# Performance work log

Measured on AMD Instinct MI355X. Metric: run time of the kernel, lower is better.

Reference implementation:

```python
import jax, jax.numpy as jnp
import numpy as np

B, H, W = 2, 64, 64
C = 19          # num_classes
D = 64          # embed_dim
NH = 4          # num_heads
E = 4           # num_experts
HD = 128        # hidden_dim = 2*D
EPS = 1e-5


def setup_inputs() -> dict:
    key = jax.random.key(0)
    ks = jax.random.split(key, 12)
    n = lambda k, shape, s=0.02: jax.random.normal(k, shape, jnp.float32) * s
    z = lambda shape: jnp.zeros(shape, jnp.float32)
    o = lambda shape: jnp.ones(shape, jnp.float32)
    return {
        "depth_map": jax.random.normal(ks[0], (B, 1, H, W), jnp.float32),
        "prob_map": jax.nn.softmax(jax.random.normal(ks[1], (B, C, H, W), jnp.float32), axis=1),
        "emb_w": n(ks[2], (1 + C, D)), "emb_b": z((D,)),            # 1x1 conv == per-pixel linear
        "in_proj_w": n(ks[3], (D, 3 * D)), "in_proj_b": z((3 * D,)),
        "attn_out_w": n(ks[4], (D, D)), "attn_out_b": z((D,)),
        "ln1_g": o((D,)), "ln1_b": z((D,)),
        "ln2_g": o((D,)), "ln2_b": z((D,)),
        "exp_w1": n(ks[5], (E, D, HD)), "exp_b1": z((E, HD)),
        "exp_w2": n(ks[6], (E, HD, D)), "exp_b2": z((E, D)),
        "gate_w": n(ks[7], (D, E)), "gate_b": z((E,)),
        "proj_w": n(ks[8], (D, 1)), "proj_b": z((1,)),
    }


def _layernorm(x, g, b):
    m = jnp.mean(x, axis=-1, keepdims=True)
    v = jnp.mean(jnp.square(x - m), axis=-1, keepdims=True)
    return (x - m) * jax.lax.rsqrt(v + EPS) * g + b


def reference(depth_map, prob_map, emb_w, emb_b, in_proj_w, in_proj_b,
              attn_out_w, attn_out_b, ln1_g, ln1_b, ln2_g, ln2_b,
              exp_w1, exp_b1, exp_w2, exp_b2, gate_w, gate_b, proj_w, proj_b):
    Bv, _, Hv, Wv = depth_map.shape
    N = Hv * Wv
    dh = D // NH

    x = jnp.concatenate([depth_map, prob_map], axis=1)            # [B, 1+C, H, W]
    # 1x1 conv embedding -> token sequence [B, N, D]
    x_seq = (jnp.einsum('bchw,cd->bhwd', x, emb_w) + emb_b).reshape(Bv, N, D)

    # pre-norm self-attention
    xn = _layernorm(x_seq, ln1_g, ln1_b)
    qkv = xn @ in_proj_w + in_proj_b                              # [B, N, 3D]
    q, k, v = jnp.split(qkv, 3, axis=-1)
    q = q.reshape(Bv, N, NH, dh)
    k = k.reshape(Bv, N, NH, dh)
    v = v.reshape(Bv, N, NH, dh)
    scores = jnp.einsum('bqhd,bkhd->bhqk', q, k) / np.sqrt(dh).astype(np.float32)
    attn = jax.nn.softmax(scores, axis=-1)
    o = jnp.einsum('bhqk,bkhd->bqhd', attn, v).reshape(Bv, N, D)
    attn_out = o @ attn_out_w + attn_out_b
    x_att = x_seq + attn_out

    # soft MoE over all tokens
    xn2 = _layernorm(x_att, ln2_g, ln2_b)
    gw = jax.nn.softmax(xn2 @ gate_w + gate_b, axis=-1)           # [B, N, E]
    h1 = jax.nn.relu(jnp.einsum('bnd,edh->bneh', xn2, exp_w1) + exp_b1)
    eo = jnp.einsum('bneh,ehd->bned', h1, exp_w2) + exp_b2        # [B, N, E, D]
    combined = jnp.einsum('bned,bne->bnd', eo, gw)
    x_out = x_att + combined

    weight_seq = x_out @ proj_w + proj_b                          # [B, N, 1]
    return jax.nn.sigmoid(weight_seq.reshape(Bv, 1, Hv, Wv))
```

## Files before the change

kernel.cpp:

```cpp
#include <hip/hip_runtime.h>
#include <math.h>

#define DEV __device__ __forceinline__

namespace {

constexpr int Bb  = 2;
constexpr int Nn  = 4096;
constexpr int Cc  = 19;
constexpr int NHh = 4;
constexpr int SEGS = 4;
constexpr float EPSv = 1e-5f;
constexpr float LOG2E = 1.4426950408889634f;

typedef __attribute__((ext_vector_type(4))) short short4v;
typedef __attribute__((ext_vector_type(8))) short short8v;
typedef __attribute__((ext_vector_type(4))) float f32x4;
typedef unsigned short ushort_t;
typedef unsigned int uint_t;

constexpr size_t QKV_F    = (size_t)Bb * Nn * 32;
constexpr size_t OFF_XSEQ = 0;
constexpr size_t OFF_XATT = OFF_XSEQ + (size_t)Bb*Nn*64;
constexpr size_t OFF_QB   = OFF_XATT + (size_t)Bb*Nn*64;
constexpr size_t OFF_KB   = OFF_QB + QKV_F;
constexpr size_t OFF_VB   = OFF_KB + QKV_F;
constexpr size_t OFF_VT   = OFF_VB + QKV_F;
constexpr size_t OFF_MP   = OFF_VT + QKV_F;
constexpr size_t OFF_LP   = OFF_MP + (size_t)Bb*NHh*SEGS*Nn;
constexpr size_t OFF_OP   = OFF_LP + (size_t)Bb*NHh*SEGS*Nn;
constexpr size_t OFF_XN2  = OFF_OP + (size_t)Bb*NHh*SEGS*Nn*16;
constexpr size_t OFF_GW   = OFF_XN2 + (size_t)Bb*Nn*32;
constexpr size_t OFF_H1   = OFF_GW + (size_t)Bb*Nn*4;
constexpr size_t OFF_W1T  = OFF_H1 + (size_t)Bb*Nn*256;
constexpr size_t OFF_W2T  = OFF_W1T + 16384;

DEV float wredsum(float x) {
  #pragma unroll
  for (int off = 32; off > 0; off >>= 1) x += __shfl_xor(x, off, 64);
  return x;
}
DEV ushort_t f2bf(float x) {
  uint_t u = __builtin_bit_cast(uint_t, x);
  u += 0x7fffu + ((u >> 16) & 1u);
  return (ushort_t)(u >> 16);
}
DEV uint_t cvtpk(float a, float b) {
  uint_t r;
  asm("v_cvt_pk_bf16_f32 %0, %1, %2" : "=v"(r) : "v"(a), "v"(b));
  return r;
}

__global__ __launch_bounds__(256) void k_wcvt(
    const float* __restrict__ w1, const float* __restrict__ w2,
    float* __restrict__ ws)
{
  const int idx = blockIdx.x * 256 + threadIdx.x;
  ushort_t* w1t = (ushort_t*)(ws + OFF_W1T);
  ushort_t* w2t = (ushort_t*)(ws + OFF_W2T);
  {
    const int col = idx >> 6, k = idx & 63;
    const int e = col >> 7, h = col & 127;
    w1t[idx] = f2bf(w1[((size_t)e * 64 + k) * 128 + h]);
  }
  {
    const int d = idx >> 9, kk = idx & 511;
    const int e = kk >> 7, h = kk & 127;
    w2t[idx] = f2bf(w2[((size_t)e * 128 + h) * 64 + d]);
  }
}

__global__ __launch_bounds__(256) void k_embed_qkv(
    const float* __restrict__ depth, const float* __restrict__ prob,
    const float* __restrict__ emb_w, const float* __restrict__ emb_b,
    const float* __restrict__ ipw,   const float* __restrict__ ipb,
    const float* __restrict__ ln1g,  const float* __restrict__ ln1b,
    float* __restrict__ ws)
{
  __shared__ float ipws[64 * 192];

  const int t = threadIdx.x;
  #pragma unroll
  for (int i = 0; i < 12; ++i) {
    const int idx = (i * 256 + t) * 4;
    *(float4*)&ipws[idx] = *(const float4*)&ipw[idx];
  }

  const int lane = t & 63;
  const int wid  = t >> 6;
  const int tok  = blockIdx.x * 4 + wid;
  const int b = tok >> 12, n = tok & (Nn - 1);
  const int d = lane;

  float acc = emb_b[d];
  acc += depth[(size_t)b * Nn + n] * emb_w[d];
  #pragma unroll
  for (int c = 0; c < Cc; ++c)
    acc += prob[((size_t)b * Cc + c) * Nn + n] * emb_w[(1 + c) * 64 + d];

  ws[OFF_XSEQ + (size_t)tok * 64 + d] = acc;

  float mean = wredsum(acc) * (1.f / 64.f);
  float diff = acc - mean;
  float var  = wredsum(diff * diff) * (1.f / 64.f);
  float xn   = diff * rsqrtf(var + EPSv) * ln1g[d] + ln1b[d];

  __syncthreads();

  float aq = ipb[d], ak = ipb[64 + d], av = ipb[128 + d];
  #pragma unroll 8
  for (int j = 0; j < 64; ++j) {
    float xj = __shfl(xn, j, 64);
    const float* wr = ipws + j * 192;
    aq = fmaf(xj, wr[d],       aq);
    ak = fmaf(xj, wr[64 + d],  ak);
    av = fmaf(xj, wr[128 + d], av);
  }
  const int h = d >> 4, dd = d & 15;
  ushort_t* qb = (ushort_t*)(ws + OFF_QB);
  ushort_t* kb = (ushort_t*)(ws + OFF_KB);
  ushort_t* vb = (ushort_t*)(ws + OFF_VB);
  const size_t base = ((size_t)(b * NHh + h) * Nn + n) * 16 + dd;
  qb[base] = f2bf(aq * 0.25f * LOG2E);
  kb[base] = f2bf(ak);
  vb[base] = f2bf(av);
}

__global__ __launch_bounds__(256) void k_transpose_v(float* __restrict__ ws)
{
  __shared__ ushort_t tile[256][17];
  const ushort_t* vb = (const ushort_t*)(ws + OFF_VB);
  ushort_t*       vt = (ushort_t*)(ws + OFF_VT);
  const int bh = blockIdx.y;
  const int n0 = blockIdx.x * 256;
  const int t  = threadIdx.x;

  const ushort_t* src = vb + ((size_t)bh * Nn + n0 + t) * 16;
  short8v r0 = *(const short8v*)(src);
  short8v r1 = *(const short8v*)(src + 8);
  #pragma unroll
  for (int i = 0; i < 8; ++i) { tile[t][i] = (ushort_t)r0[i]; tile[t][8 + i] = (ushort_t)r1[i]; }
  __syncthreads();

  const int d = t & 15, seg = t >> 4;
  short8v w0, w1;
  #pragma unroll
  for (int i = 0; i < 8; ++i) {
    w0[i] = (short)tile[seg * 16 + i][d];
    w1[i] = (short)tile[seg * 16 + 8 + i][d];
  }
  ushort_t* dst = vt + ((size_t)bh * 16 + d) * Nn + n0 + seg * 16;
  *(short8v*)(dst)     = w0;
  *(short8v*)(dst + 8) = w1;
}

__global__ __launch_bounds__(256, 4) void k_attn_mfma(float* __restrict__ ws)
{
  const int lane = threadIdx.x & 63;
  const int wid  = threadIdx.x >> 6;
  const int blk  = blockIdx.x;
  const int seg  = blockIdx.y;
  const int bh   = blk >> 6;
  const int qt   = (blk & 63) * 4 + wid;
  const int q0   = qt * 16;
  const int g    = lane >> 4;
  const int qi   = lane & 15;

  const ushort_t* qb = (const ushort_t*)(ws + OFF_QB) + (size_t)bh * Nn * 16;
  const ushort_t* kb = (const ushort_t*)(ws + OFF_KB) + (size_t)bh * Nn * 16;
  const ushort_t* vt = (const ushort_t*)(ws + OFF_VT) + (size_t)bh * 16 * Nn;

  short8v qf = {};
  if (lane < 32)
    qf = *(const short8v*)(qb + (size_t)(q0 + qi) * 16 + g * 8);

  f32x4 O = {0.f, 0.f, 0.f, 0.f};
  float mrun = -INFINITY;
  float lacc[4] = {0.f, 0.f, 0.f, 0.f};
  const f32x4 z4 = {0.f, 0.f, 0.f, 0.f};
  const ushort_t* vrow = vt + (size_t)qi * Nn;

  const int c0 = seg * (Nn / 64 / SEGS);
  #pragma unroll 2
  for (int c = c0; c < c0 + Nn / 64 / SEGS; ++c) {
    const int kb0 = c * 64;
    short8v kf0 = {}, kf1 = {}, kf2 = {}, kf3 = {};
    if (lane < 32) {
      const ushort_t* kr = kb + (size_t)(kb0 + qi) * 16 + g * 8;
      kf0 = *(const short8v*)(kr);
      kf1 = *(const short8v*)(kr + 256);
      kf2 = *(const short8v*)(kr + 512);
      kf3 = *(const short8v*)(kr + 768);
    }
    const ushort_t* vr = vrow + kb0 + 4 * g;
    short4v va00 = *(const short4v*)(vr);
    short4v va01 = *(const short4v*)(vr + 16);
    short4v va10 = *(const short4v*)(vr + 32);
    short4v va11 = *(const short4v*)(vr + 48);

    f32x4 s0 = __builtin_amdgcn_mfma_f32_16x16x32_bf16(kf0, qf, z4, 0, 0, 0);
    f32x4 s1 = __builtin_amdgcn_mfma_f32_16x16x32_bf16(kf1, qf, z4, 0, 0, 0);
    f32x4 s2 = __builtin_amdgcn_mfma_f32_16x16x32_bf16(kf2, qf, z4, 0, 0, 0);
    f32x4 s3 = __builtin_amdgcn_mfma_f32_16x16x32_bf16(kf3, qf, z4, 0, 0, 0);

    float lmax = fmaxf(fmaxf(fmaxf(s0[0], s0[1]), fmaxf(s0[2], s0[3])),
                       fmaxf(fmaxf(s1[0], s1[1]), fmaxf(s1[2], s1[3])));
    lmax = fmaxf(lmax, fmaxf(fmaxf(s2[0], s2[1]), fmaxf(s2[2], s2[3])));
    lmax = fmaxf(lmax, fmaxf(fmaxf(s3[0], s3[1]), fmaxf(s3[2], s3[3])));

    if (!__all(lmax <= mrun + 11.5f)) {
      float cm = lmax;
      cm = fmaxf(cm, __shfl_xor(cm, 16, 64));
      cm = fmaxf(cm, __shfl_xor(cm, 32, 64));
      const float nm = fmaxf(mrun, cm);
      const float c2 = exp2f(mrun - nm);
      lacc[0] *= c2; lacc[1] *= c2; lacc[2] *= c2; lacc[3] *= c2;
      O[0] *= c2; O[1] *= c2; O[2] *= c2; O[3] *= c2;
      mrun = nm;
    }

    float p[16];
    #pragma unroll
    for (int r = 0; r < 4; ++r) {
      p[r]      = exp2f(s0[r] - mrun);
      p[4 + r]  = exp2f(s1[r] - mrun);
      p[8 + r]  = exp2f(s2[r] - mrun);
      p[12 + r] = exp2f(s3[r] - mrun);
    }
    #pragma unroll
    for (int i = 0; i < 16; ++i) lacc[i & 3] += p[i];

    union { short8v v; uint_t w[4]; } P0, P1;
    P0.w[0] = cvtpk(p[0], p[1]);   P0.w[1] = cvtpk(p[2], p[3]);
    P0.w[2] = cvtpk(p[4], p[5]);   P0.w[3] = cvtpk(p[6], p[7]);
    P1.w[0] = cvtpk(p[8], p[9]);   P1.w[1] = cvtpk(p[10], p[11]);
    P1.w[2] = cvtpk(p[12], p[13]); P1.w[3] = cvtpk(p[14], p[15]);

    union { short8v v; short4v hh[2]; } VA0, VA1;
    VA0.hh[0] = va00; VA0.hh[1] = va01;
    VA1.hh[0] = va10; VA1.hh[1] = va11;

    O = __builtin_amdgcn_mfma_f32_16x16x32_bf16(VA0.v, P0.v, O, 0, 0, 0);
    O = __builtin_amdgcn_mfma_f32_16x16x32_bf16(VA1.v, P1.v, O, 0, 0, 0);
  }

  float lrun = ((lacc[0] + lacc[1]) + (lacc[2] + lacc[3]));
  lrun += __shfl_xor(lrun, 16, 64);
  lrun += __shfl_xor(lrun, 32, 64);

  const size_t pb = ((size_t)bh * SEGS + seg) * Nn + q0 + qi;
  if (g == 0) { ws[OFF_MP + pb] = mrun; ws[OFF_LP + pb] = lrun; }
  f32x4* op = (f32x4*)(ws + OFF_OP + pb * 16 + g * 4);
  *op = O;
}

__global__ __launch_bounds__(256) void k_out_ln2(
    const float* __restrict__ aow,  const float* __restrict__ aob,
    const float* __restrict__ ln2g, const float* __restrict__ ln2b,
    const float* __restrict__ gwt,  const float* __restrict__ gbt,
    float* __restrict__ ws)
{
  __shared__ float aows[64 * 64];
  const int t = threadIdx.x;
  #pragma unroll
  for (int i = 0; i < 4; ++i) {
    const int idx = (i * 256 + t) * 4;
    *(float4*)&aows[idx] = *(const float4*)&aow[idx];
  }

  const int lane = t & 63;
  const int wid  = t >> 6;
  const int tok  = blockIdx.x * 4 + wid;
  const int b = tok >> 12, n = tok & (Nn - 1);
  const int h = lane >> 4, dd = lane & 15;
  const int bh = b * NHh + h;

  float M = -INFINITY;
  #pragma unroll
  for (int s = 0; s < SEGS; ++s)
    M = fmaxf(M, ws[OFF_MP + ((size_t)bh * SEGS + s) * Nn + n]);
  float L = 0.f, oa = 0.f;
  #pragma unroll
  for (int s = 0; s < SEGS; ++s) {
    const size_t pb = ((size_t)bh * SEGS + s) * Nn + n;
    const float c = exp2f(ws[OFF_MP + pb] - M);
    L  = fmaf(ws[OFF_LP + pb], c, L);
    oa = fmaf(ws[OFF_OP + pb * 16 + dd], c, oa);
  }
  const float o = oa / L;

  __syncthreads();

  float acc = aob[lane];
  #pragma unroll 8
  for (int j = 0; j < 64; ++j)
    acc = fmaf(__shfl(o, j, 64), aows[j * 64 + lane], acc);
  const size_t xi = (size_t)tok * 64 + lane;
  const float xa = ws[OFF_XSEQ + xi] + acc;
  ws[OFF_XATT + xi] = xa;

  float mean = wredsum(xa) * (1.f / 64.f);
  float diff = xa - mean;
  float var  = wredsum(diff * diff) * (1.f / 64.f);
  float xn   = diff * rsqrtf(var + EPSv) * ln2g[lane] + ln2b[lane];

  ushort_t* xn2 = (ushort_t*)(ws + OFF_XN2);
  xn2[xi] = f2bf(xn);

  float ge[4];
  #pragma unroll
  for (int e = 0; e < 4; ++e) ge[e] = xn * gwt[lane * 4 + e];
  #pragma unroll
  for (int off = 32; off > 0; off >>= 1) {
    #pragma unroll
    for (int e = 0; e < 4; ++e) ge[e] += __shfl_xor(ge[e], off, 64);
  }
  #pragma unroll
  for (int e = 0; e < 4; ++e) ge[e] += gbt[e];
  float gm = fmaxf(fmaxf(ge[0], ge[1]), fmaxf(ge[2], ge[3]));
  float gs = 0.f;
  #pragma unroll
  for (int e = 0; e < 4; ++e) { ge[e] = __expf(ge[e] - gm); gs += ge[e]; }
  if (lane == 0) {
    float* gw = ws + OFF_GW + (size_t)tok * 4;
    #pragma unroll
    for (int e = 0; e < 4; ++e) gw[e] = ge[e] / gs;
  }
}

__global__ __launch_bounds__(256) void k_gemm1(
    const float* __restrict__ eb1, float* __restrict__ ws)
{
  const int lane = threadIdx.x & 63;
  const int wid  = threadIdx.x >> 6;
  const int qi = lane & 15, g = lane >> 4;
  const int tok0 = blockIdx.x * 64 + wid * 16;
  const int col0 = blockIdx.y * 64;

  const ushort_t* xn2 = (const ushort_t*)(ws + OFF_XN2);
  const ushort_t* w1t = (const ushort_t*)(ws + OFF_W1T);
  const float* gw = ws + OFF_GW;
  ushort_t* h1 = (ushort_t*)(ws + OFF_H1);

  const short8v a0 = *(const short8v*)(xn2 + (size_t)(tok0 + qi) * 64 + g * 8);
  const short8v a1 = *(const short8v*)(xn2 + (size_t)(tok0 + qi) * 64 + 32 + g * 8);

  f32x4 acc[4] = {{0,0,0,0},{0,0,0,0},{0,0,0,0},{0,0,0,0}};
  #pragma unroll
  for (int cf = 0; cf < 4; ++cf) {
    const int col = col0 + cf * 16 + qi;
    const short8v b0 = *(const short8v*)(w1t + (size_t)col * 64 + g * 8);
    const short8v b1 = *(const short8v*)(w1t + (size_t)col * 64 + 32 + g * 8);
    acc[cf] = __builtin_amdgcn_mfma_f32_16x16x32_bf16(a0, b0, acc[cf], 0, 0, 0);
    acc[cf] = __builtin_amdgcn_mfma_f32_16x16x32_bf16(a1, b1, acc[cf], 0, 0, 0);
  }
  #pragma unroll
  for (int cf = 0; cf < 4; ++cf) {
    const int col = col0 + cf * 16 + qi;
    const int e = col >> 7;
    const float bb = eb1[col];
    #pragma unroll
    for (int r = 0; r < 4; ++r) {
      const int tok = tok0 + g * 4 + r;
      float v = fmaxf(acc[cf][r] + bb, 0.f) * gw[(size_t)tok * 4 + e];
      h1[(size_t)tok * 512 + col] = f2bf(v);
    }
  }
}

__global__ __launch_bounds__(64) void k_gemm2f(
    const float* __restrict__ b2, const float* __restrict__ pw,
    const float* __restrict__ pbv, const float* __restrict__ ws,
    float* __restrict__ out)
{
  const int lane = threadIdx.x;
  const int qi = lane & 15, g = lane >> 4;
  const int tok0 = blockIdx.x * 16;

  const ushort_t* h1  = (const ushort_t*)(ws + OFF_H1);
  const ushort_t* w2t = (const ushort_t*)(ws + OFF_W2T);

  f32x4 acc[4] = {{0,0,0,0},{0,0,0,0},{0,0,0,0},{0,0,0,0}};
  #pragma unroll 4
  for (int s = 0; s < 16; ++s) {
    const short8v a = *(const short8v*)(h1 + (size_t)(tok0 + qi) * 512 + s * 32 + g * 8);
    #pragma unroll
    for (int cf = 0; cf < 4; ++cf) {
      const short8v b = *(const short8v*)(w2t + (size_t)(cf * 16 + qi) * 512 + s * 32 + g * 8);
      acc[cf] = __builtin_amdgcn_mfma_f32_16x16x32_bf16(a, b, acc[cf], 0, 0, 0);
    }
  }

  const float* xatt = ws + OFF_XATT;
  const float* gw   = ws + OFF_GW;

  float gwv[4][4];
  #pragma unroll
  for (int r = 0; r < 4; ++r) {
    const int tok = tok0 + g * 4 + r;
    #pragma unroll
    for (int e = 0; e < 4; ++e) gwv[r][e] = gw[(size_t)tok * 4 + e];
  }

  float part[4] = {0.f, 0.f, 0.f, 0.f};
  #pragma unroll
  for (int cf = 0; cf < 4; ++cf) {
    const int d = cf * 16 + qi;
    const float pwd = pw[d];
    const float b20 = b2[d], b21 = b2[64 + d], b22 = b2[128 + d], b23 = b2[192 + d];
    #pragma unroll
    for (int r = 0; r < 4; ++r) {
      const int tok = tok0 + g * 4 + r;
      const float bias2 = gwv[r][0]*b20 + gwv[r][1]*b21 + gwv[r][2]*b22 + gwv[r][3]*b23;
      const float xo = xatt[(size_t)tok * 64 + d] + acc[cf][r] + bias2;
      part[r] = fmaf(xo, pwd, part[r]);
    }
  }
  #pragma unroll
  for (int r = 0; r < 4; ++r) {
    #pragma unroll
    for (int mask = 8; mask > 0; mask >>= 1)
      part[r] += __shfl_xor(part[r], mask, 64);
  }
  if (qi == 0) {
    const float pb0 = pbv[0];
    #pragma unroll
    for (int r = 0; r < 4; ++r)
      out[tok0 + g * 4 + r] = 1.f / (1.f + __expf(-(part[r] + pb0)));
  }
}

}

extern "C" void kernel_launch(void* const* d_in, const int* in_sizes, int n_in,
                              void* d_out, int out_size, void* d_ws, size_t ws_size,
                              hipStream_t stream) {
  const float* depth = (const float*)d_in[0];
  const float* prob  = (const float*)d_in[1];
  const float* emb_w = (const float*)d_in[2];
  const float* emb_b = (const float*)d_in[3];
  const float* ipw   = (const float*)d_in[4];
  const float* ipb   = (const float*)d_in[5];
  const float* aow   = (const float*)d_in[6];
  const float* aob   = (const float*)d_in[7];
  const float* ln1g  = (const float*)d_in[8];
  const float* ln1b  = (const float*)d_in[9];
  const float* ln2g  = (const float*)d_in[10];
  const float* ln2b  = (const float*)d_in[11];
  const float* w1    = (const float*)d_in[12];
  const float* b1    = (const float*)d_in[13];
  const float* w2    = (const float*)d_in[14];
  const float* b2    = (const float*)d_in[15];
  const float* gatew = (const float*)d_in[16];
  const float* gateb = (const float*)d_in[17];
  const float* projw = (const float*)d_in[18];
  const float* projb = (const float*)d_in[19];
  float* out = (float*)d_out;
  float* wsf = (float*)d_ws;

  k_wcvt<<<128, 256, 0, stream>>>(w1, w2, wsf);
  k_embed_qkv<<<Bb * Nn / 4, 256, 0, stream>>>(depth, prob, emb_w, emb_b,
                                               ipw, ipb, ln1g, ln1b, wsf);
  k_transpose_v<<<dim3(Nn / 256, Bb * NHh), 256, 0, stream>>>(wsf);
  k_attn_mfma<<<dim3(Bb * NHh * 64, SEGS), 256, 0, stream>>>(wsf);
  k_out_ln2<<<Bb * Nn / 4, 256, 0, stream>>>(aow, aob, ln2g, ln2b,
                                             gatew, gateb, wsf);
  k_gemm1<<<dim3(Bb * Nn / 64, 8), 256, 0, stream>>>(b1, wsf);
  k_gemm2f<<<Bb * Nn / 16, 64, 0, stream>>>(b2, projw, projb, wsf, out);
}
```

Baseline: 231.7 us.

## Fuse MoE expert GEMMs via shared-memory hidden tile, merge weight conversion, halve attention segments

Merges the two expert GEMM kernels into one, so the gated hidden activations for 32 tokens are kept in shared memory instead of being written to and re-read from global memory. Folds the bf16 weight transpose/convert into the embedding kernel to drop a launch. Also reduces the attention key-split count from 4 to 2, which shrinks the partial-result buffers and merge work but lowers grid parallelism. The fused kernel adds block-level syncs and uses a large shared-memory tile, which may limit occupancy.

```diff
diff --git a/kernel.cpp b/kernel.cpp
--- a/kernel.cpp
+++ b/kernel.cpp
@@ -9,7 +9,7 @@
 constexpr int Nn  = 4096;
 constexpr int Cc  = 19;
 constexpr int NHh = 4;
-constexpr int SEGS = 4;
+constexpr int SEGS = 2;
 constexpr float EPSv = 1e-5f;
 constexpr float LOG2E = 1.4426950408889634f;
 
@@ -31,8 +31,7 @@
 constexpr size_t OFF_OP   = OFF_LP + (size_t)Bb*NHh*SEGS*Nn;
 constexpr size_t OFF_XN2  = OFF_OP + (size_t)Bb*NHh*SEGS*Nn*16;
 constexpr size_t OFF_GW   = OFF_XN2 + (size_t)Bb*Nn*32;
-constexpr size_t OFF_H1   = OFF_GW + (size_t)Bb*Nn*4;
-constexpr size_t OFF_W1T  = OFF_H1 + (size_t)Bb*Nn*256;
+constexpr size_t OFF_W1T  = OFF_GW + (size_t)Bb*Nn*4;
 constexpr size_t OFF_W2T  = OFF_W1T + 16384;
 
 DEV float wredsum(float x) {
@@ -49,25 +48,6 @@
   uint_t r;
   asm("v_cvt_pk_bf16_f32 %0, %1, %2" : "=v"(r) : "v"(a), "v"(b));
   return r;
-}
-
-__global__ __launch_bounds__(256) void k_wcvt(
-    const float* __restrict__ w1, const float* __restrict__ w2,
-    float* __restrict__ ws)
-{
-  const int idx = blockIdx.x * 256 + threadIdx.x;
-  ushort_t* w1t = (ushort_t*)(ws + OFF_W1T);
-  ushort_t* w2t = (ushort_t*)(ws + OFF_W2T);
-  {
-    const int col = idx >> 6, k = idx & 63;
-    const int e = col >> 7, h = col & 127;
-    w1t[idx] = f2bf(w1[((size_t)e * 64 + k) * 128 + h]);
-  }
-  {
-    const int d = idx >> 9, kk = idx & 511;
-    const int e = kk >> 7, h = kk & 127;
-    w2t[idx] = f2bf(w2[((size_t)e * 128 + h) * 64 + d]);
-  }
 }
 
 __global__ __launch_bounds__(256) void k_embed_qkv(
@@ -75,11 +55,29 @@
     const float* __restrict__ emb_w, const float* __restrict__ emb_b,
     const float* __restrict__ ipw,   const float* __restrict__ ipb,
     const float* __restrict__ ln1g,  const float* __restrict__ ln1b,
+    const float* __restrict__ w1,    const float* __restrict__ w2,
     float* __restrict__ ws)
 {
   __shared__ float ipws[64 * 192];
 
   const int t = threadIdx.x;
+
+  if (blockIdx.x < 128) {
+    const int idx = blockIdx.x * 256 + t;
+    ushort_t* w1t = (ushort_t*)(ws + OFF_W1T);
+    ushort_t* w2t = (ushort_t*)(ws + OFF_W2T);
+    {
+      const int col = idx >> 6, k = idx & 63;
+      const int e = col >> 7, h = col & 127;
+      w1t[idx] = f2bf(w1[((size_t)e * 64 + k) * 128 + h]);
+    }
+    {
+      const int d = idx >> 9, kk = idx & 511;
+      const int e = kk >> 7, h = kk & 127;
+      w2t[idx] = f2bf(w2[((size_t)e * 128 + h) * 64 + d]);
+    }
+  }
+
   #pragma unroll
   for (int i = 0; i < 12; ++i) {
     const int idx = (i * 256 + t) * 4;
@@ -328,91 +326,82 @@
   }
 }
 
-__global__ __launch_bounds__(256) void k_gemm1(
-    const float* __restrict__ eb1, float* __restrict__ ws)
+__global__ __launch_bounds__(256) void k_moe2(
+    const float* __restrict__ eb1, const float* __restrict__ b2,
+    const float* __restrict__ pw,  const float* __restrict__ pbv,
+    float* __restrict__ ws,        float* __restrict__ out)
 {
-  const int lane = threadIdx.x & 63;
-  const int wid  = threadIdx.x >> 6;
+  __shared__ ushort_t h1s[32][520];
+  __shared__ float gws[32][4];
+  __shared__ float partial[32][2];
+
+  const int t = threadIdx.x;
+  const int lane = t & 63, wid = t >> 6;
   const int qi = lane & 15, g = lane >> 4;
-  const int tok0 = blockIdx.x * 64 + wid * 16;
-  const int col0 = blockIdx.y * 64;
+  const int tokB = blockIdx.x * 32;
+
+  if (t < 128)
+    gws[t >> 2][t & 3] = ws[OFF_GW + (size_t)(tokB + (t >> 2)) * 4 + (t & 3)];
+
+  const int th   = wid >> 1;
+  const int tok0 = tokB + th * 16;
+  const int col0 = (wid & 1) * 256;
 
   const ushort_t* xn2 = (const ushort_t*)(ws + OFF_XN2);
   const ushort_t* w1t = (const ushort_t*)(ws + OFF_W1T);
-  const float* gw = ws + OFF_GW;
-  ushort_t* h1 = (ushort_t*)(ws + OFF_H1);
+  const ushort_t* w2t = (const ushort_t*)(ws + OFF_W2T);
 
   const short8v a0 = *(const short8v*)(xn2 + (size_t)(tok0 + qi) * 64 + g * 8);
   const short8v a1 = *(const short8v*)(xn2 + (size_t)(tok0 + qi) * 64 + 32 + g * 8);
 
-  f32x4 acc[4] = {{0,0,0,0},{0,0,0,0},{0,0,0,0},{0,0,0,0}};
-  #pragma unroll
-  for (int cf = 0; cf < 4; ++cf) {
+  __syncthreads();
+
+  const f32x4 z4 = {0.f, 0.f, 0.f, 0.f};
+  #pragma unroll 4
+  for (int cf = 0; cf < 16; ++cf) {
     const int col = col0 + cf * 16 + qi;
     const short8v b0 = *(const short8v*)(w1t + (size_t)col * 64 + g * 8);
     const short8v b1 = *(const short8v*)(w1t + (size_t)col * 64 + 32 + g * 8);
-    acc[cf] = __builtin_amdgcn_mfma_f32_16x16x32_bf16(a0, b0, acc[cf], 0, 0, 0);
-    acc[cf] = __builtin_amdgcn_mfma_f32_16x16x32_bf16(a1, b1, acc[cf], 0, 0, 0);
-  }
-  #pragma unroll
-  for (int cf = 0; cf < 4; ++cf) {
-    const int col = col0 + cf * 16 + qi;
+    f32x4 acc = __builtin_amdgcn_mfma_f32_16x16x32_bf16(a0, b0, z4, 0, 0, 0);
+    acc = __builtin_amdgcn_mfma_f32_16x16x32_bf16(a1, b1, acc, 0, 0, 0);
     const int e = col >> 7;
     const float bb = eb1[col];
     #pragma unroll
     for (int r = 0; r < 4; ++r) {
-      const int tok = tok0 + g * 4 + r;
-      float v = fmaxf(acc[cf][r] + bb, 0.f) * gw[(size_t)tok * 4 + e];
-      h1[(size_t)tok * 512 + col] = f2bf(v);
-    }
-  }
-}
-
-__global__ __launch_bounds__(64) void k_gemm2f(
-    const float* __restrict__ b2, const float* __restrict__ pw,
-    const float* __restrict__ pbv, const float* __restrict__ ws,
-    float* __restrict__ out)
-{
-  const int lane = threadIdx.x;
-  const int qi = lane & 15, g = lane >> 4;
-  const int tok0 = blockIdx.x * 16;
-
-  const ushort_t* h1  = (const ushort_t*)(ws + OFF_H1);
-  const ushort_t* w2t = (const ushort_t*)(ws + OFF_W2T);
-
-  f32x4 acc[4] = {{0,0,0,0},{0,0,0,0},{0,0,0,0},{0,0,0,0}};
+      const int ltok = th * 16 + g * 4 + r;
+      const float v = fmaxf(acc[r] + bb, 0.f) * gws[ltok][e];
+      h1s[ltok][col] = f2bf(v);
+    }
+  }
+
+  __syncthreads();
+
+  const int dbase = (wid & 1) * 32;
+  f32x4 acc2[2] = {{0,0,0,0},{0,0,0,0}};
   #pragma unroll 4
   for (int s = 0; s < 16; ++s) {
-    const short8v a = *(const short8v*)(h1 + (size_t)(tok0 + qi) * 512 + s * 32 + g * 8);
-    #pragma unroll
-    for (int cf = 0; cf < 4; ++cf) {
-      const short8v b = *(const short8v*)(w2t + (size_t)(cf * 16 + qi) * 512 + s * 32 + g * 8);
-      acc[cf] = __builtin_amdgcn_mfma_f32_16x16x32_bf16(a, b, acc[cf], 0, 0, 0);
+    const short8v a = *(const short8v*)&h1s[th * 16 + qi][s * 32 + g * 8];
+    #pragma unroll
+    for (int df = 0; df < 2; ++df) {
+      const int d = dbase + df * 16 + qi;
+      const short8v b = *(const short8v*)(w2t + (size_t)d * 512 + s * 32 + g * 8);
+      acc2[df] = __builtin_amdgcn_mfma_f32_16x16x32_bf16(a, b, acc2[df], 0, 0, 0);
     }
   }
 
   const float* xatt = ws + OFF_XATT;
-  const float* gw   = ws + OFF_GW;
-
-  float gwv[4][4];
-  #pragma unroll
-  for (int r = 0; r < 4; ++r) {
-    const int tok = tok0 + g * 4 + r;
-    #pragma unroll
-    for (int e = 0; e < 4; ++e) gwv[r][e] = gw[(size_t)tok * 4 + e];
-  }
-
   float part[4] = {0.f, 0.f, 0.f, 0.f};
   #pragma unroll
-  for (int cf = 0; cf < 4; ++cf) {
-    const int d = cf * 16 + qi;
+  for (int df = 0; df < 2; ++df) {
+    const int d = dbase + df * 16 + qi;
     const float pwd = pw[d];
     const float b20 = b2[d], b21 = b2[64 + d], b22 = b2[128 + d], b23 = b2[192 + d];
     #pragma unroll
     for (int r = 0; r < 4; ++r) {
-      const int tok = tok0 + g * 4 + r;
-      const float bias2 = gwv[r][0]*b20 + gwv[r][1]*b21 + gwv[r][2]*b22 + gwv[r][3]*b23;
-      const float xo = xatt[(size_t)tok * 64 + d] + acc[cf][r] + bias2;
+      const int ltok = th * 16 + g * 4 + r;
+      const float* gwr = gws[ltok];
+      const float bias2 = gwr[0]*b20 + gwr[1]*b21 + gwr[2]*b22 + gwr[3]*b23;
+      const float xo = xatt[(size_t)(tokB + ltok) * 64 + d] + acc2[df][r] + bias2;
       part[r] = fmaf(xo, pwd, part[r]);
     }
   }
@@ -423,10 +412,14 @@
       part[r] += __shfl_xor(part[r], mask, 64);
   }
   if (qi == 0) {
-    const float pb0 = pbv[0];
     #pragma unroll
     for (int r = 0; r < 4; ++r)
-      out[tok0 + g * 4 + r] = 1.f / (1.f + __expf(-(part[r] + pb0)));
+      partial[th * 16 + g * 4 + r][wid & 1] = part[r];
+  }
+  __syncthreads();
+  if (t < 32) {
+    const float v = partial[t][0] + partial[t][1] + 0.f;
+    out[tokB + t] = 1.f / (1.f + __expf(-(v + pbv[0])));
   }
 }
 
@@ -458,13 +451,11 @@
   float* out = (float*)d_out;
   float* wsf = (float*)d_ws;
 
-  k_wcvt<<<128, 256, 0, stream>>>(w1, w2, wsf);
   k_embed_qkv<<<Bb * Nn / 4, 256, 0, stream>>>(depth, prob, emb_w, emb_b,
-                                               ipw, ipb, ln1g, ln1b, wsf);
+                                               ipw, ipb, ln1g, ln1b, w1, w2, wsf);
   k_transpose_v<<<dim3(Nn / 256, Bb * NHh), 256, 0, stream>>>(wsf);
   k_attn_mfma<<<dim3(Bb * NHh * 64, SEGS), 256, 0, stream>>>(wsf);
   k_out_ln2<<<Bb * Nn / 4, 256, 0, stream>>>(aow, aob, ln2g, ln2b,
                                              gatew, gateb, wsf);
-  k_gemm1<<<dim3(Bb * Nn / 64, 8), 256, 0, stream>>>(b1, wsf);
-  k_gemm2f<<<Bb * Nn / 16, 64, 0, stream>>>(b2, projw, projb, wsf, out);
-}
+  k_moe2<<<Bb * Nn / 32, 256, 0, stream>>>(b1, b2, projw, projb, wsf, out);
+}
```

Result: faster. 213.0 us (-8.1%).
